# Optimization experiments

Hardware: AMD Instinct MI355X
Metric: run time of the kernel (lower is better)

## Reference

```python
import jax, jax.numpy as jnp
import numpy as np

N = 50000
E = 800000
EPS = 1e-12


def sage_conv(x, src, dst, W_l, b_l, W_r):
    # PyG SAGEConv (mean aggr): out = lin_l(mean_{j in N(i)} x_j) + lin_r(x_i)
    msg = x[src]                                             # [E, d] gather
    agg = jax.ops.segment_sum(msg, dst, num_segments=N)      # [N, d]
    cnt = jax.ops.segment_sum(jnp.ones((E,), x.dtype), dst, num_segments=N)
    mean = agg / jnp.maximum(cnt, 1.0)[:, None]              # isolated nodes -> 0
    return mean @ W_l + b_l + x @ W_r


def setup_inputs() -> dict:
    key = jax.random.key(0)
    ks = jax.random.split(key, 12)
    s = 0.05
    return {
        "x": jax.random.normal(ks[0], (N, 128), dtype=jnp.float32),
        "edge_index": jax.random.randint(ks[1], (2, E), 0, N, dtype=jnp.int64),
        # pre: Linear(128 -> 128)
        "pre_W": jax.random.normal(ks[2], (128, 128), dtype=jnp.float32) * s,
        "pre_b": jnp.zeros((128,), dtype=jnp.float32),
        # conv_first: SAGEConv(128 -> 256)
        "W1_l": jax.random.normal(ks[3], (128, 256), dtype=jnp.float32) * s,
        "b1": jnp.zeros((256,), dtype=jnp.float32),
        "W1_r": jax.random.normal(ks[4], (128, 256), dtype=jnp.float32) * s,
        # conv_hidden[0]: SAGEConv(256 -> 256)
        "W2_l": jax.random.normal(ks[5], (256, 256), dtype=jnp.float32) * s,
        "b2": jnp.zeros((256,), dtype=jnp.float32),
        "W2_r": jax.random.normal(ks[6], (256, 256), dtype=jnp.float32) * s,
        # conv_out: SAGEConv(256 -> 256)
        "W3_l": jax.random.normal(ks[7], (256, 256), dtype=jnp.float32) * s,
        "b3": jnp.zeros((256,), dtype=jnp.float32),
        "W3_r": jax.random.normal(ks[8], (256, 256), dtype=jnp.float32) * s,
    }


def reference(x, edge_index, pre_W, pre_b, W1_l, b1, W1_r, W2_l, b2, W2_r, W3_l, b3, W3_r):
    src, dst = edge_index[0], edge_index[1]
    h = x @ pre_W + pre_b                                   # feature_pre Linear
    h = jax.nn.relu(sage_conv(h, src, dst, W1_l, b1, W1_r))  # dropout = identity (eval)
    h = jax.nn.relu(sage_conv(h, src, dst, W2_l, b2, W2_r))
    h = sage_conv(h, src, dst, W3_l, b3, W3_r)
    norm = jnp.sqrt(jnp.sum(h * h, axis=-1, keepdims=True))
    return h / jnp.maximum(norm, EPS)                       # F.normalize(p=2, dim=-1)
```

## Files before the change

kernel.cpp:

```cpp
#include <hip/hip_runtime.h>
#include <cstddef>
#include <cstdint>


typedef __attribute__((ext_vector_type(8))) short short8;
typedef __attribute__((ext_vector_type(4))) float f32x4;
typedef __attribute__((ext_vector_type(2))) float f32x2;

__device__ __forceinline__ unsigned rne_bf16(float f) {
    unsigned b = __float_as_uint(f);
    return (b + 0x7fffu + ((b >> 16) & 1u)) >> 16;
}
__device__ __forceinline__ float bf16_lo(unsigned u) { return __uint_as_float(u << 16); }
__device__ __forceinline__ float bf16_hi(unsigned u) { return __uint_as_float(u & 0xffff0000u); }


__device__ __forceinline__ float dec_e4m3_sw(unsigned v) {
    unsigned s = (v & 0x80u) << 24;
    unsigned em = v & 0x7fu;
    float out;
    if (em < 8u) {
        out = (float)em * 0.001953125f;
    } else {
        out = __uint_as_float((((em >> 3) + 120u) << 23) | ((em & 7u) << 20));
    }
    return __uint_as_float(__float_as_uint(out) | s);
}

__device__ __forceinline__ unsigned char enc_e4m3(float f) {
#if __has_builtin(__builtin_amdgcn_cvt_pk_fp8_f32)
    return (unsigned char)(__builtin_amdgcn_cvt_pk_fp8_f32(f, f, 0, false) & 0xff);
#else
    unsigned b = __float_as_uint(f);
    unsigned s = (b >> 24) & 0x80u;
    unsigned a = b & 0x7fffffffu;
    if (a >= 0x43E00000u) return (unsigned char)(s | 0x7Eu);
    if (a < 0x3C800000u) {
        unsigned m = (unsigned)rintf(__uint_as_float(a) * 512.0f);
        return (unsigned char)(s | m);
    }
    unsigned r = a + 0x7FFFFu + ((a >> 20) & 1u);
    unsigned E8 = (r >> 23) - 120u;
    unsigned M = (r >> 20) & 7u;
    if (E8 > 15u || (E8 == 15u && M == 7u)) return (unsigned char)(s | 0x7Eu);
    return (unsigned char)(s | (E8 << 3) | M);
#endif
}

__device__ __forceinline__ void acc16(float* a, uint4 u) {
#if __has_builtin(__builtin_amdgcn_cvt_pk_f32_fp8)
    f32x2 f;
    f = __builtin_amdgcn_cvt_pk_f32_fp8(u.x, false); a[0] += f.x;  a[1] += f.y;
    f = __builtin_amdgcn_cvt_pk_f32_fp8(u.x, true);  a[2] += f.x;  a[3] += f.y;
    f = __builtin_amdgcn_cvt_pk_f32_fp8(u.y, false); a[4] += f.x;  a[5] += f.y;
    f = __builtin_amdgcn_cvt_pk_f32_fp8(u.y, true);  a[6] += f.x;  a[7] += f.y;
    f = __builtin_amdgcn_cvt_pk_f32_fp8(u.z, false); a[8] += f.x;  a[9] += f.y;
    f = __builtin_amdgcn_cvt_pk_f32_fp8(u.z, true);  a[10] += f.x; a[11] += f.y;
    f = __builtin_amdgcn_cvt_pk_f32_fp8(u.w, false); a[12] += f.x; a[13] += f.y;
    f = __builtin_amdgcn_cvt_pk_f32_fp8(u.w, true);  a[14] += f.x; a[15] += f.y;
#else
    unsigned d0 = u.x, d1 = u.y, d2 = u.z, d3 = u.w;
#pragma unroll
    for (int t = 0; t < 4; ++t) a[t]      += dec_e4m3_sw((d0 >> (8 * t)) & 0xffu);
#pragma unroll
    for (int t = 0; t < 4; ++t) a[4 + t]  += dec_e4m3_sw((d1 >> (8 * t)) & 0xffu);
#pragma unroll
    for (int t = 0; t < 4; ++t) a[8 + t]  += dec_e4m3_sw((d2 >> (8 * t)) & 0xffu);
#pragma unroll
    for (int t = 0; t < 4; ++t) a[12 + t] += dec_e4m3_sw((d3 >> (8 * t)) & 0xffu);
#endif
}

__device__ __forceinline__ void stage16(const void* g, unsigned short* ldsbase,
                                        int lane) {
#if __has_builtin(__builtin_amdgcn_global_load_lds)
    (void)lane;
    __builtin_amdgcn_global_load_lds(
        (const __attribute__((address_space(1))) unsigned int*)g,
        (__attribute__((address_space(3))) unsigned int*)ldsbase, 16, 0, 0);
#else
    *(uint4*)(ldsbase + (size_t)lane * 8) = *(const uint4*)g;
#endif
}


__global__ __launch_bounds__(256) void deg_kernel(const int* __restrict__ dst,
                                                  int* __restrict__ deg, int E) {
    int e = blockIdx.x * 256 + threadIdx.x;
    if (e < E) atomicAdd(&deg[dst[e]], 1);
}

__global__ __launch_bounds__(256) void bsum_kernel(const int* __restrict__ deg,
                                                   int* __restrict__ bsum, int n) {
    int i = blockIdx.x * 256 + threadIdx.x;
    int v = (i < n) ? deg[i] : 0;
#pragma unroll
    for (int s = 32; s > 0; s >>= 1) v += __shfl_down(v, s);
    __shared__ int ws[4];
    int lane = threadIdx.x & 63, w = threadIdx.x >> 6;
    if (lane == 0) ws[w] = v;
    __syncthreads();
    if (threadIdx.x == 0) bsum[blockIdx.x] = ws[0] + ws[1] + ws[2] + ws[3];
}

__global__ __launch_bounds__(256) void bscan_kernel(const int* __restrict__ bsum,
                                                    int* __restrict__ boff,
                                                    int* __restrict__ off,
                                                    int nb, int n, int E) {
    int t = threadIdx.x;
    int v = (t < nb) ? bsum[t] : 0;
    int incl = v;
#pragma unroll
    for (int s = 1; s < 64; s <<= 1) {
        int u = __shfl_up(incl, s);
        if ((t & 63) >= s) incl += u;
    }
    __shared__ int ws[4];
    int lane = t & 63, w = t >> 6;
    if (lane == 63) ws[w] = incl;
    __syncthreads();
    int woff = 0;
    for (int j = 0; j < w; ++j) woff += ws[j];
    if (t < nb) boff[t] = woff + incl - v;
    if (t == 0) off[n] = E;
}

__global__ __launch_bounds__(256) void scan_kernel(const int* __restrict__ deg,
                                                   const int* __restrict__ boff,
                                                   int* __restrict__ off,
                                                   float* __restrict__ inv, int n) {
    int i = blockIdx.x * 256 + threadIdx.x;
    int v = (i < n) ? deg[i] : 0;
    int incl = v;
#pragma unroll
    for (int s = 1; s < 64; s <<= 1) {
        int u = __shfl_up(incl, s);
        if ((threadIdx.x & 63) >= s) incl += u;
    }
    __shared__ int ws[4];
    int lane = threadIdx.x & 63, w = threadIdx.x >> 6;
    if (lane == 63) ws[w] = incl;
    __syncthreads();
    int woff = 0;
    for (int j = 0; j < w; ++j) woff += ws[j];
    if (i < n) {
        off[i] = boff[blockIdx.x] + woff + incl - v;
        inv[i] = 1.0f / fmaxf((float)v, 1.0f);
    }
}


__global__ __launch_bounds__(256) void prep_all(
    const float* __restrict__ x, uint2* __restrict__ xb, int n4, int XB,
    const float* __restrict__ pre_W, const float* __restrict__ W1_l,
    const float* __restrict__ W1_r, const float* __restrict__ W2_l,
    const float* __restrict__ W2_r, const float* __restrict__ W3_l,
    const float* __restrict__ W3_r,
    unsigned short* __restrict__ WT0, unsigned short* __restrict__ WT1,
    unsigned short* __restrict__ WT2, unsigned short* __restrict__ WT3,
    unsigned short* __restrict__ WT4, unsigned short* __restrict__ WT5,
    unsigned short* __restrict__ WT6) {
    if (blockIdx.x < (unsigned)XB) {
        int i = blockIdx.x * 256 + threadIdx.x;
        if (i >= n4) return;
        float4 v = ((const float4*)x)[i];
        uint2 o;
        o.x = rne_bf16(v.x) | (rne_bf16(v.y) << 16);
        o.y = rne_bf16(v.z) | (rne_bf16(v.w) << 16);
        xb[i] = o;
        return;
    }
    int idx = (blockIdx.x - XB) * 256 + threadIdx.x;
    if (idx < 16384) {
        int k = idx >> 7, n = idx & 127;
        WT0[n * 128 + k] = (unsigned short)rne_bf16(pre_W[idx]);
        return;
    }
    idx -= 16384;
    if (idx < 32768) {
        int k = idx >> 8, n = idx & 255;
        WT1[n * 128 + k] = (unsigned short)rne_bf16(W1_l[idx]);
        return;
    }
    idx -= 32768;
    if (idx < 32768) {
        int k = idx >> 8, n = idx & 255;
        WT2[n * 128 + k] = (unsigned short)rne_bf16(W1_r[idx]);
        return;
    }
    idx -= 32768;
    if (idx < 65536) {
        int k = idx >> 8, n = idx & 255;
        WT3[n * 256 + k] = (unsigned short)rne_bf16(W2_l[idx]);
        return;
    }
    idx -= 65536;
    if (idx < 65536) {
        int k = idx >> 8, n = idx & 255;
        WT4[n * 256 + k] = (unsigned short)rne_bf16(W2_r[idx]);
        return;
    }
    idx -= 65536;
    if (idx < 65536) {
        int k = idx >> 8, n = idx & 255;
        WT5[n * 256 + k] = (unsigned short)rne_bf16(W3_l[idx]);
        return;
    }
    idx -= 65536;
    if (idx < 65536) {
        int k = idx >> 8, n = idx & 255;
        WT6[n * 256 + k] = (unsigned short)rne_bf16(W3_r[idx]);
    }
}


template <int D>
__global__ __launch_bounds__(256) void gather_b(const unsigned short* __restrict__ h,
                                                const int* __restrict__ off,
                                                const int* __restrict__ ssrc,
                                                const float* __restrict__ inv,
                                                unsigned short* __restrict__ agg, int n) {
    int node = blockIdx.x * 4 + (threadIdx.x >> 6);
    if (node >= n) return;
    int lane = threadIdx.x & 63;
    int beg = off[node], end = off[node + 1];
    float sc = inv[node];

    const int q   = lane >> 4;
    const int sub = lane & 15;
    const unsigned short* col = h + (sub << 3);
    float a[8] = {0, 0, 0, 0, 0, 0, 0, 0};
    float b[8] = {0, 0, 0, 0, 0, 0, 0, 0};
    int k = beg;
    for (; k + 7 < end; k += 8) {
        int s0 = ssrc[k + q];
        int s1 = ssrc[k + 4 + q];
        uint4 u = *(const uint4*)(col + (size_t)s0 * D);
        uint4 v = *(const uint4*)(col + (size_t)s1 * D);
        a[0] += bf16_lo(u.x); a[1] += bf16_hi(u.x);
        a[2] += bf16_lo(u.y); a[3] += bf16_hi(u.y);
        a[4] += bf16_lo(u.z); a[5] += bf16_hi(u.z);
        a[6] += bf16_lo(u.w); a[7] += bf16_hi(u.w);
        b[0] += bf16_lo(v.x); b[1] += bf16_hi(v.x);
        b[2] += bf16_lo(v.y); b[3] += bf16_hi(v.y);
        b[4] += bf16_lo(v.z); b[5] += bf16_hi(v.z);
        b[6] += bf16_lo(v.w); b[7] += bf16_hi(v.w);
    }
    for (; k < end; k += 4) {
        int e = k + q;
        if (e < end) {
            uint4 u = *(const uint4*)(col + (size_t)ssrc[e] * D);
            a[0] += bf16_lo(u.x); a[1] += bf16_hi(u.x);
            a[2] += bf16_lo(u.y); a[3] += bf16_hi(u.y);
            a[4] += bf16_lo(u.z); a[5] += bf16_hi(u.z);
            a[6] += bf16_lo(u.w); a[7] += bf16_hi(u.w);
        }
    }
#pragma unroll
    for (int i = 0; i < 8; ++i) a[i] += b[i];
#pragma unroll
    for (int i = 0; i < 8; ++i) a[i] += __shfl_xor(a[i], 16);
#pragma unroll
    for (int i = 0; i < 8; ++i) a[i] += __shfl_xor(a[i], 32);
    if (q == 0) {
#pragma unroll
        for (int i = 0; i < 8; ++i) a[i] *= sc;
        uint4 o;
        o.x = rne_bf16(a[0]) | (rne_bf16(a[1]) << 16);
        o.y = rne_bf16(a[2]) | (rne_bf16(a[3]) << 16);
        o.z = rne_bf16(a[4]) | (rne_bf16(a[5]) << 16);
        o.w = rne_bf16(a[6]) | (rne_bf16(a[7]) << 16);
        *(uint4*)(agg + (size_t)node * D + (sub << 3)) = o;
    }
}


__global__ __launch_bounds__(256) void gather8(const unsigned char* __restrict__ h8,
                                               const int* __restrict__ off,
                                               const int* __restrict__ ssrc,
                                               const float* __restrict__ inv,
                                               unsigned short* __restrict__ agg, int n) {
    int node = blockIdx.x * 4 + (threadIdx.x >> 6);
    if (node >= n) return;
    int lane = threadIdx.x & 63;
    const int q   = lane >> 4;
    const int sub = lane & 15;
    int beg = off[node], end = off[node + 1];
    float sc = inv[node];
    const unsigned char* col = h8 + (sub << 4);

    float a[16], b[16];
#pragma unroll
    for (int i = 0; i < 16; ++i) { a[i] = 0.f; b[i] = 0.f; }

    int k = beg;
    for (; k + 7 < end; k += 8) {
        int s0 = ssrc[k + q];
        int s1 = ssrc[k + 4 + q];
        uint4 u = *(const uint4*)(col + (size_t)s0 * 256);
        uint4 v = *(const uint4*)(col + (size_t)s1 * 256);
        acc16(a, u);
        acc16(b, v);
    }
    for (; k < end; k += 4) {
        int e = k + q;
        if (e < end) {
            uint4 u = *(const uint4*)(col + (size_t)ssrc[e] * 256);
            acc16(a, u);
        }
    }
#pragma unroll
    for (int i = 0; i < 16; ++i) a[i] += b[i];
#pragma unroll
    for (int i = 0; i < 16; ++i) a[i] += __shfl_xor(a[i], 16);
#pragma unroll
    for (int i = 0; i < 16; ++i) a[i] += __shfl_xor(a[i], 32);
    if (q == 0) {
#pragma unroll
        for (int i = 0; i < 16; ++i) a[i] *= sc;
        uint4 o1, o2;
        o1.x = rne_bf16(a[0])  | (rne_bf16(a[1])  << 16);
        o1.y = rne_bf16(a[2])  | (rne_bf16(a[3])  << 16);
        o1.z = rne_bf16(a[4])  | (rne_bf16(a[5])  << 16);
        o1.w = rne_bf16(a[6])  | (rne_bf16(a[7])  << 16);
        o2.x = rne_bf16(a[8])  | (rne_bf16(a[9])  << 16);
        o2.y = rne_bf16(a[10]) | (rne_bf16(a[11]) << 16);
        o2.z = rne_bf16(a[12]) | (rne_bf16(a[13]) << 16);
        o2.w = rne_bf16(a[14]) | (rne_bf16(a[15]) << 16);
        *(uint4*)(agg + (size_t)node * 256 + (sub << 4)) = o1;
        *(uint4*)(agg + (size_t)node * 256 + (sub << 4) + 8) = o2;
    }
}


__global__ __launch_bounds__(256) void fatB(
    const unsigned short* __restrict__ xb, const unsigned short* __restrict__ WT0,
    const float* __restrict__ pre_b, unsigned short* __restrict__ h0b, int M,
    int GB,
    const int* __restrict__ src, const int* __restrict__ dst,
    const int* __restrict__ off, int* __restrict__ deg,
    int* __restrict__ ssrc, int E) {
    __shared__ __align__(16) unsigned short As[64 * 64];

    if (blockIdx.x >= (unsigned)GB) {
        int e = (blockIdx.x - GB) * 256 + threadIdx.x;
        if (e >= E) return;
        int d = dst[e];
        int pos = off[d] + atomicSub(&deg[d], 1) - 1;
        ssrc[pos] = src[e];
        return;
    }

    const int t = threadIdx.x;
    const int lane = t & 63;
    const int w = t >> 6;
    const int wm = w >> 1, wn = w & 1;
    const int m0 = blockIdx.x * 64;
    const int K = 128;

    f32x4 acc[2][4];
#pragma unroll
    for (int i = 0; i < 2; ++i)
#pragma unroll
        for (int j = 0; j < 4; ++j) acc[i][j] = (f32x4){0.f, 0.f, 0.f, 0.f};

    for (int k0 = 0; k0 < K; k0 += 64) {
#pragma unroll
        for (int i = 0; i < 2; ++i) {
            int base = (w * 2 + i) * 64;
            int p = base + lane;
            int row = p >> 3, slot = p & 7;
            int c = slot ^ (row & 7);
            int gm = m0 + row;
            if (gm >= M) gm = M - 1;
            stage16(xb + (size_t)gm * K + k0 + c * 8, &As[(size_t)base * 8], lane);
        }
        __syncthreads();
#pragma unroll
        for (int kk = 0; kk < 2; ++kk) {
            int ac = kk * 4 + (lane >> 4);
            short8 af[2], bfr[4];
#pragma unroll
            for (int i = 0; i < 2; ++i) {
                int arow = wm * 32 + i * 16 + (lane & 15);
                af[i] = *(const short8*)&As[arow * 64 + ((ac ^ (arow & 7)) << 3)];
            }
#pragma unroll
            for (int i = 0; i < 4; ++i) {
                int brow = wn * 64 + i * 16 + (lane & 15);
                bfr[i] = *(const short8*)(WT0 + (size_t)brow * K + k0 + ac * 8);
            }
#pragma unroll
            for (int mi = 0; mi < 2; ++mi)
#pragma unroll
                for (int ni = 0; ni < 4; ++ni)
                    acc[mi][ni] = __builtin_amdgcn_mfma_f32_16x16x32_bf16(
                        af[mi], bfr[ni], acc[mi][ni], 0, 0, 0);
        }
        __syncthreads();
    }

#pragma unroll
    for (int ni = 0; ni < 4; ++ni) {
        int n = wn * 64 + ni * 16 + (lane & 15);
        float bv = pre_b[n];
#pragma unroll
        for (int mi = 0; mi < 2; ++mi) {
            int mbase = m0 + wm * 32 + mi * 16 + ((lane >> 4) << 2);
#pragma unroll
            for (int r = 0; r < 4; ++r) {
                int m = mbase + r;
                if (m >= M) continue;
                h0b[(size_t)m * 128 + n] = (unsigned short)rne_bf16(acc[mi][ni][r] + bv);
            }
        }
    }
}

__global__ __launch_bounds__(256) void gemm_wide(
    const unsigned short* __restrict__ A1, const unsigned short* __restrict__ W1T,
    const unsigned short* __restrict__ A2, const unsigned short* __restrict__ W2T,
    const float* __restrict__ bias,
    unsigned short* __restrict__ outb, unsigned char* __restrict__ out8,
    float* __restrict__ outf, int M, int K, int relu) {
    __shared__ __align__(16) unsigned short As[64 * 64];
    __shared__ float rs[64][4];

    const int t = threadIdx.x;
    const int lane = t & 63;
    const int w = t >> 6;
    const int m0 = blockIdx.x * 64;

    f32x4 acc[4][4];
#pragma unroll
    for (int i = 0; i < 4; ++i)
#pragma unroll
        for (int j = 0; j < 4; ++j) acc[i][j] = (f32x4){0.f, 0.f, 0.f, 0.f};

    for (int pass = 0; pass < 2; ++pass) {
        const unsigned short* A = pass ? A2 : A1;
        const unsigned short* W = pass ? W2T : W1T;

        for (int k0 = 0; k0 < K; k0 += 64) {
#pragma unroll
            for (int i = 0; i < 2; ++i) {
                int base = (w * 2 + i) * 64;
                int p = base + lane;
                int row = p >> 3, slot = p & 7;
                int c = slot ^ (row & 7);
                int gm = m0 + row;
                if (gm >= M) gm = M - 1;
                stage16(A + (size_t)gm * K + k0 + c * 8, &As[(size_t)base * 8], lane);
            }
            __syncthreads();
#pragma unroll
            for (int kk = 0; kk < 2; ++kk) {
                int ac = kk * 4 + (lane >> 4);
                short8 af[4], bfr[4];
#pragma unroll
                for (int i = 0; i < 4; ++i) {
                    int arow = i * 16 + (lane & 15);
                    af[i] = *(const short8*)&As[arow * 64 + ((ac ^ (arow & 7)) << 3)];
                    int brow = w * 64 + i * 16 + (lane & 15);
                    bfr[i] = *(const short8*)(W + (size_t)brow * K + k0 + ac * 8);
                }
#pragma unroll
                for (int mi = 0; mi < 4; ++mi)
#pragma unroll
                    for (int ni = 0; ni < 4; ++ni)
                        acc[mi][ni] = __builtin_amdgcn_mfma_f32_16x16x32_bf16(
                            af[mi], bfr[ni], acc[mi][ni], 0, 0, 0);
            }
            __syncthreads();
        }
    }

    if (outb) {
#pragma unroll
        for (int ni = 0; ni < 4; ++ni) {
            int n = w * 64 + ni * 16 + (lane & 15);
            float bv = bias[n];
#pragma unroll
            for (int mi = 0; mi < 4; ++mi) {
                int mbase = m0 + mi * 16 + ((lane >> 4) << 2);
#pragma unroll
                for (int r = 0; r < 4; ++r) {
                    int m = mbase + r;
                    if (m >= M) continue;
                    float v = acc[mi][ni][r] + bv;
                    if (relu) v = fmaxf(v, 0.0f);
                    outb[(size_t)m * 256 + n] = (unsigned short)rne_bf16(v);
                    if (out8) out8[(size_t)m * 256 + n] = enc_e4m3(v);
                }
            }
        }
        return;
    }

#pragma unroll
    for (int ni = 0; ni < 4; ++ni) {
        float bv = bias[w * 64 + ni * 16 + (lane & 15)];
#pragma unroll
        for (int mi = 0; mi < 4; ++mi)
#pragma unroll
            for (int r = 0; r < 4; ++r) acc[mi][ni][r] += bv;
    }
#pragma unroll
    for (int mi = 0; mi < 4; ++mi) {
#pragma unroll
        for (int r = 0; r < 4; ++r) {
            float p = acc[mi][0][r] * acc[mi][0][r] + acc[mi][1][r] * acc[mi][1][r] +
                      acc[mi][2][r] * acc[mi][2][r] + acc[mi][3][r] * acc[mi][3][r];
            p += __shfl_xor(p, 1);
            p += __shfl_xor(p, 2);
            p += __shfl_xor(p, 4);
            p += __shfl_xor(p, 8);
            if ((lane & 15) == 0)
                rs[mi * 16 + ((lane >> 4) << 2) + r][w] = p;
        }
    }
    __syncthreads();
#pragma unroll
    for (int mi = 0; mi < 4; ++mi) {
        int lrow0 = mi * 16 + ((lane >> 4) << 2);
#pragma unroll
        for (int r = 0; r < 4; ++r) {
            int m = m0 + lrow0 + r;
            if (m >= M) continue;
            float s = rs[lrow0 + r][0] + rs[lrow0 + r][1] + rs[lrow0 + r][2] + rs[lrow0 + r][3];
            float sc = 1.0f / fmaxf(sqrtf(s), 1e-12f);
#pragma unroll
            for (int ni = 0; ni < 4; ++ni) {
                int n = w * 64 + ni * 16 + (lane & 15);
                outf[(size_t)m * 256 + n] = acc[mi][ni][r] * sc;
            }
        }
    }
}

extern "C" void kernel_launch(void* const* d_in, const int* in_sizes, int n_in,
                              void* d_out, int out_size, void* d_ws, size_t ws_size,
                              hipStream_t stream) {
    const int N = 50000;
    const int E = 800000;
    const int NB = (N + 255) / 256;

    const float* x     = (const float*)d_in[0];
    const int*   ei    = (const int*)d_in[1];
    const float* pre_W = (const float*)d_in[2];
    const float* pre_b = (const float*)d_in[3];
    const float* W1_l  = (const float*)d_in[4];
    const float* b1    = (const float*)d_in[5];
    const float* W1_r  = (const float*)d_in[6];
    const float* W2_l  = (const float*)d_in[7];
    const float* b2    = (const float*)d_in[8];
    const float* W2_r  = (const float*)d_in[9];
    const float* W3_l  = (const float*)d_in[10];
    const float* b3    = (const float*)d_in[11];
    const float* W3_r  = (const float*)d_in[12];
    float* out = (float*)d_out;

    const int* src = ei;
    const int* dst = ei + E;

    int* deg  = (int*)d_ws;
    int* off  = deg + N;
    int* bsum = off + N + 1;
    int* boff = bsum + 256;
    int* ssrc = boff + 256;
    size_t int_words = (size_t)2 * N + 1 + 512 + E;
    int_words = (int_words + 3) & ~(size_t)3;

    float* inv = (float*)d_ws + int_words;
    unsigned short* us = (unsigned short*)(inv + N);

    unsigned short* xb  = us;                 us += (size_t)N * 128;
    unsigned short* WT0 = us;                 us += 16384;
    unsigned short* WT1 = us;                 us += 32768;
    unsigned short* WT2 = us;                 us += 32768;
    unsigned short* WT3 = us;                 us += 65536;
    unsigned short* WT4 = us;                 us += 65536;
    unsigned short* WT5 = us;                 us += 65536;
    unsigned short* WT6 = us;                 us += 65536;
    unsigned short* h0b   = us;               us += (size_t)N * 128;
    unsigned short* agg1b = us;               us += (size_t)N * 128;
    unsigned short* h1b   = us;               us += (size_t)N * 256;
    unsigned short* agg2b = us;               us += (size_t)N * 256;
    unsigned short* h2b   = us;               us += (size_t)N * 256;
    unsigned short* agg3b = us;               us += (size_t)N * 256;
    unsigned char* h1f8 = (unsigned char*)us;
    unsigned char* h2f8 = h1f8 + (size_t)N * 256;

    hipMemsetAsync(deg, 0, (size_t)N * sizeof(int), stream);
    deg_kernel<<<(E + 255) / 256, 256, 0, stream>>>(dst, deg, E);
    bsum_kernel<<<NB, 256, 0, stream>>>(deg, bsum, N);
    bscan_kernel<<<1, 256, 0, stream>>>(bsum, boff, off, NB, N, E);
    scan_kernel<<<NB, 256, 0, stream>>>(deg, boff, off, inv, N);

    const int n4 = N * 128 / 4;
    const int XB = (n4 + 255) / 256;
    const int WB = (344064 + 255) / 256;
    prep_all<<<XB + WB, 256, 0, stream>>>(x, (uint2*)xb, n4, XB,
                                          pre_W, W1_l, W1_r, W2_l, W2_r, W3_l,
                                          W3_r, WT0, WT1, WT2, WT3, WT4, WT5, WT6);

    const int MT2 = (N + 63) / 64;
    const int AG = (N + 3) / 4;
    const int DB = (E + 255) / 256;

    fatB<<<MT2 + DB, 256, 0, stream>>>(xb, WT0, pre_b, h0b, N, MT2,
                                       src, dst, off, deg, ssrc, E);

    gather_b<128><<<AG, 256, 0, stream>>>(h0b, off, ssrc, inv, agg1b, N);
    gemm_wide<<<MT2, 256, 0, stream>>>(agg1b, WT1, h0b, WT2, b1,
                                       h1b, h1f8, nullptr, N, 128, 1);

    gather8<<<AG, 256, 0, stream>>>(h1f8, off, ssrc, inv, agg2b, N);
    gemm_wide<<<MT2, 256, 0, stream>>>(agg2b, WT3, h1b, WT4, b2,
                                       h2b, h2f8, nullptr, N, 256, 1);

    gather8<<<AG, 256, 0, stream>>>(h2f8, off, ssrc, inv, agg3b, N);
    gemm_wide<<<MT2, 256, 0, stream>>>(agg3b, WT5, h2b, WT6, b3,
                                       nullptr, nullptr, out, N, 256, 0);
}
```

Measured before the change: 496.7 us.

## Fuse degree count into prep, use 16-bit CSR indices, LDS-stage weights in wider GEMM

Three unrelated changes. The degree-count atomics move into the bf16 prep kernel, saving one launch. The CSR source indices are stored as 16-bit values, halving index traffic in the gather kernels; this is exact only because N=50000 fits in 16 bits. gemm_wide now uses 512-thread blocks over 128 rows and stages weight tiles into LDS instead of reading them from global memory per wave. The trade is more LDS per block and fewer blocks in flight.

```diff
diff --git a/kernel.cpp b/kernel.cpp
--- a/kernel.cpp
+++ b/kernel.cpp
@@ -84,12 +84,6 @@
 }
 
 
-__global__ __launch_bounds__(256) void deg_kernel(const int* __restrict__ dst,
-                                                  int* __restrict__ deg, int E) {
-    int e = blockIdx.x * 256 + threadIdx.x;
-    if (e < E) atomicAdd(&deg[dst[e]], 1);
-}
-
 __global__ __launch_bounds__(256) void bsum_kernel(const int* __restrict__ deg,
                                                    int* __restrict__ bsum, int n) {
     int i = blockIdx.x * 256 + threadIdx.x;
@@ -150,8 +144,8 @@
 }
 
 
-__global__ __launch_bounds__(256) void prep_all(
-    const float* __restrict__ x, uint2* __restrict__ xb, int n4, int XB,
+__global__ __launch_bounds__(256) void fatA(
+    const float* __restrict__ x, uint2* __restrict__ xb, int n4, int XB, int PB,
     const float* __restrict__ pre_W, const float* __restrict__ W1_l,
     const float* __restrict__ W1_r, const float* __restrict__ W2_l,
     const float* __restrict__ W2_r, const float* __restrict__ W3_l,
@@ -159,7 +153,13 @@
     unsigned short* __restrict__ WT0, unsigned short* __restrict__ WT1,
     unsigned short* __restrict__ WT2, unsigned short* __restrict__ WT3,
     unsigned short* __restrict__ WT4, unsigned short* __restrict__ WT5,
-    unsigned short* __restrict__ WT6) {
+    unsigned short* __restrict__ WT6,
+    const int* __restrict__ dst, int* __restrict__ deg, int E) {
+    if (blockIdx.x >= (unsigned)PB) {
+        int e = (blockIdx.x - PB) * 256 + threadIdx.x;
+        if (e < E) atomicAdd(&deg[dst[e]], 1);
+        return;
+    }
     if (blockIdx.x < (unsigned)XB) {
         int i = blockIdx.x * 256 + threadIdx.x;
         if (i >= n4) return;
@@ -217,7 +217,7 @@
 template <int D>
 __global__ __launch_bounds__(256) void gather_b(const unsigned short* __restrict__ h,
                                                 const int* __restrict__ off,
-                                                const int* __restrict__ ssrc,
+                                                const unsigned short* __restrict__ ssrc16,
                                                 const float* __restrict__ inv,
                                                 unsigned short* __restrict__ agg, int n) {
     int node = blockIdx.x * 4 + (threadIdx.x >> 6);
@@ -233,8 +233,8 @@
     float b[8] = {0, 0, 0, 0, 0, 0, 0, 0};
     int k = beg;
     for (; k + 7 < end; k += 8) {
-        int s0 = ssrc[k + q];
-        int s1 = ssrc[k + 4 + q];
+        int s0 = ssrc16[k + q];
+        int s1 = ssrc16[k + 4 + q];
         uint4 u = *(const uint4*)(col + (size_t)s0 * D);
         uint4 v = *(const uint4*)(col + (size_t)s1 * D);
         a[0] += bf16_lo(u.x); a[1] += bf16_hi(u.x);
@@ -249,7 +249,7 @@
     for (; k < end; k += 4) {
         int e = k + q;
         if (e < end) {
-            uint4 u = *(const uint4*)(col + (size_t)ssrc[e] * D);
+            uint4 u = *(const uint4*)(col + (size_t)ssrc16[e] * D);
             a[0] += bf16_lo(u.x); a[1] += bf16_hi(u.x);
             a[2] += bf16_lo(u.y); a[3] += bf16_hi(u.y);
             a[4] += bf16_lo(u.z); a[5] += bf16_hi(u.z);
@@ -277,7 +277,7 @@
 
 __global__ __launch_bounds__(256) void gather8(const unsigned char* __restrict__ h8,
                                                const int* __restrict__ off,
-                                               const int* __restrict__ ssrc,
+                                               const unsigned short* __restrict__ ssrc16,
                                                const float* __restrict__ inv,
                                                unsigned short* __restrict__ agg, int n) {
     int node = blockIdx.x * 4 + (threadIdx.x >> 6);
@@ -295,8 +295,8 @@
 
     int k = beg;
     for (; k + 7 < end; k += 8) {
-        int s0 = ssrc[k + q];
-        int s1 = ssrc[k + 4 + q];
+        int s0 = ssrc16[k + q];
+        int s1 = ssrc16[k + 4 + q];
         uint4 u = *(const uint4*)(col + (size_t)s0 * 256);
         uint4 v = *(const uint4*)(col + (size_t)s1 * 256);
         acc16(a, u);
@@ -305,7 +305,7 @@
     for (; k < end; k += 4) {
         int e = k + q;
         if (e < end) {
-            uint4 u = *(const uint4*)(col + (size_t)ssrc[e] * 256);
+            uint4 u = *(const uint4*)(col + (size_t)ssrc16[e] * 256);
             acc16(a, u);
         }
     }
@@ -339,7 +339,7 @@
     int GB,
     const int* __restrict__ src, const int* __restrict__ dst,
     const int* __restrict__ off, int* __restrict__ deg,
-    int* __restrict__ ssrc, int E) {
+    unsigned short* __restrict__ ssrc16, int E) {
     __shared__ __align__(16) unsigned short As[64 * 64];
 
     if (blockIdx.x >= (unsigned)GB) {
@@ -347,7 +347,7 @@
         if (e >= E) return;
         int d = dst[e];
         int pos = off[d] + atomicSub(&deg[d], 1) - 1;
-        ssrc[pos] = src[e];
+        ssrc16[pos] = (unsigned short)src[e];
         return;
     }
 
@@ -417,19 +417,21 @@
     }
 }
 
-__global__ __launch_bounds__(256) void gemm_wide(
+__global__ __launch_bounds__(512) void gemm_wide(
     const unsigned short* __restrict__ A1, const unsigned short* __restrict__ W1T,
     const unsigned short* __restrict__ A2, const unsigned short* __restrict__ W2T,
     const float* __restrict__ bias,
     unsigned short* __restrict__ outb, unsigned char* __restrict__ out8,
     float* __restrict__ outf, int M, int K, int relu) {
-    __shared__ __align__(16) unsigned short As[64 * 64];
-    __shared__ float rs[64][4];
+    __shared__ __align__(16) unsigned short As[128 * 64];
+    __shared__ __align__(16) unsigned short Bs[256 * 64];
+    __shared__ float rs[128][4];
 
     const int t = threadIdx.x;
     const int lane = t & 63;
-    const int w = t >> 6;
-    const int m0 = blockIdx.x * 64;
+    const int w8 = t >> 6;
+    const int wm = w8 >> 2, wn = w8 & 3;
+    const int m0 = blockIdx.x * 128;
 
     f32x4 acc[4][4];
 #pragma unroll
@@ -444,7 +446,7 @@
         for (int k0 = 0; k0 < K; k0 += 64) {
 #pragma unroll
             for (int i = 0; i < 2; ++i) {
-                int base = (w * 2 + i) * 64;
+                int base = (w8 * 2 + i) * 64;
                 int p = base + lane;
                 int row = p >> 3, slot = p & 7;
                 int c = slot ^ (row & 7);
@@ -452,17 +454,25 @@
                 if (gm >= M) gm = M - 1;
                 stage16(A + (size_t)gm * K + k0 + c * 8, &As[(size_t)base * 8], lane);
             }
+#pragma unroll
+            for (int i = 0; i < 4; ++i) {
+                int base = (w8 * 4 + i) * 64;
+                int p = base + lane;
+                int row = p >> 3, slot = p & 7;
+                int c = slot ^ (row & 7);
+                stage16(W + (size_t)row * K + k0 + c * 8, &Bs[(size_t)base * 8], lane);
+            }
             __syncthreads();
 #pragma unroll
             for (int kk = 0; kk < 2; ++kk) {
+                short8 af[4], bfr[4];
                 int ac = kk * 4 + (lane >> 4);
-                short8 af[4], bfr[4];
 #pragma unroll
                 for (int i = 0; i < 4; ++i) {
-                    int arow = i * 16 + (lane & 15);
+                    int arow = wm * 64 + i * 16 + (lane & 15);
                     af[i] = *(const short8*)&As[arow * 64 + ((ac ^ (arow & 7)) << 3)];
-                    int brow = w * 64 + i * 16 + (lane & 15);
-                    bfr[i] = *(const short8*)(W + (size_t)brow * K + k0 + ac * 8);
+                    int brow = wn * 64 + i * 16 + (lane & 15);
+                    bfr[i] = *(const short8*)&Bs[brow * 64 + ((ac ^ (brow & 7)) << 3)];
                 }
 #pragma unroll
                 for (int mi = 0; mi < 4; ++mi)
@@ -478,11 +488,11 @@
     if (outb) {
 #pragma unroll
         for (int ni = 0; ni < 4; ++ni) {
-            int n = w * 64 + ni * 16 + (lane & 15);
+            int n = wn * 64 + ni * 16 + (lane & 15);
             float bv = bias[n];
 #pragma unroll
             for (int mi = 0; mi < 4; ++mi) {
-                int mbase = m0 + mi * 16 + ((lane >> 4) << 2);
+                int mbase = m0 + wm * 64 + mi * 16 + ((lane >> 4) << 2);
 #pragma unroll
                 for (int r = 0; r < 4; ++r) {
                     int m = mbase + r;
@@ -499,7 +509,7 @@
 
 #pragma unroll
     for (int ni = 0; ni < 4; ++ni) {
-        float bv = bias[w * 64 + ni * 16 + (lane & 15)];
+        float bv = bias[wn * 64 + ni * 16 + (lane & 15)];
 #pragma unroll
         for (int mi = 0; mi < 4; ++mi)
 #pragma unroll
@@ -516,22 +526,23 @@
             p += __shfl_xor(p, 4);
             p += __shfl_xor(p, 8);
             if ((lane & 15) == 0)
-                rs[mi * 16 + ((lane >> 4) << 2) + r][w] = p;
+                rs[wm * 64 + mi * 16 + ((lane >> 4) << 2) + r][wn] = p;
         }
     }
     __syncthreads();
 #pragma unroll
     for (int mi = 0; mi < 4; ++mi) {
-        int lrow0 = mi * 16 + ((lane >> 4) << 2);
+        int mbase = m0 + wm * 64 + mi * 16 + ((lane >> 4) << 2);
+        int lrow = wm * 64 + mi * 16 + ((lane >> 4) << 2);
 #pragma unroll
         for (int r = 0; r < 4; ++r) {
-            int m = m0 + lrow0 + r;
+            int m = mbase + r;
             if (m >= M) continue;
-            float s = rs[lrow0 + r][0] + rs[lrow0 + r][1] + rs[lrow0 + r][2] + rs[lrow0 + r][3];
+            float s = rs[lrow + r][0] + rs[lrow + r][1] + rs[lrow + r][2] + rs[lrow + r][3];
             float sc = 1.0f / fmaxf(sqrtf(s), 1e-12f);
 #pragma unroll
             for (int ni = 0; ni < 4; ++ni) {
-                int n = w * 64 + ni * 16 + (lane & 15);
+                int n = wn * 64 + ni * 16 + (lane & 15);
                 outf[(size_t)m * 256 + n] = acc[mi][ni][r] * sc;
             }
         }
@@ -567,8 +578,8 @@
     int* off  = deg + N;
     int* bsum = off + N + 1;
     int* boff = bsum + 256;
-    int* ssrc = boff + 256;
-    size_t int_words = (size_t)2 * N + 1 + 512 + E;
+    unsigned short* ssrc16 = (unsigned short*)(boff + 256);
+    size_t int_words = (size_t)2 * N + 1 + 512 + E / 2;
     int_words = (int_words + 3) & ~(size_t)3;
 
     float* inv = (float*)d_ws + int_words;
@@ -591,35 +602,36 @@
     unsigned char* h1f8 = (unsigned char*)us;
     unsigned char* h2f8 = h1f8 + (size_t)N * 256;
 
+    const int n4 = N * 128 / 4;
+    const int XB = (n4 + 255) / 256;
+    const int WB = (344064 + 255) / 256;
+    const int PB = XB + WB;
+    const int DB = (E + 255) / 256;
+    const int MT  = (N + 127) / 128;
+    const int MT2 = (N + 63) / 64;
+    const int AG = (N + 3) / 4;
+
     hipMemsetAsync(deg, 0, (size_t)N * sizeof(int), stream);
-    deg_kernel<<<(E + 255) / 256, 256, 0, stream>>>(dst, deg, E);
+    fatA<<<PB + DB, 256, 0, stream>>>(x, (uint2*)xb, n4, XB, PB,
+                                      pre_W, W1_l, W1_r, W2_l, W2_r, W3_l, W3_r,
+                                      WT0, WT1, WT2, WT3, WT4, WT5, WT6,
+                                      dst, deg, E);
     bsum_kernel<<<NB, 256, 0, stream>>>(deg, bsum, N);
     bscan_kernel<<<1, 256, 0, stream>>>(bsum, boff, off, NB, N, E);
     scan_kernel<<<NB, 256, 0, stream>>>(deg, boff, off, inv, N);
 
-    const int n4 = N * 128 / 4;
-    const int XB = (n4 + 255) / 256;
-    const int WB = (344064 + 255) / 256;
-    prep_all<<<XB + WB, 256, 0, stream>>>(x, (uint2*)xb, n4, XB,
-                                          pre_W, W1_l, W1_r, W2_l, W2_r, W3_l,
-                                          W3_r, WT0, WT1, WT2, WT3, WT4, WT5, WT6);
-
-    const int MT2 = (N + 63) / 64;
-    const int AG = (N + 3) / 4;
-    const int DB = (E + 255) / 256;
-
     fatB<<<MT2 + DB, 256, 0, stream>>>(xb, WT0, pre_b, h0b, N, MT2,
-                                       src, dst, off, deg, ssrc, E);
-
-    gather_b<128><<<AG, 256, 0, stream>>>(h0b, off, ssrc, inv, agg1b, N);
-    gemm_wide<<<MT2, 256, 0, stream>>>(agg1b, WT1, h0b, WT2, b1,
-                                       h1b, h1f8, nullptr, N, 128, 1);
-
-    gather8<<<AG, 256, 0, stream>>>(h1f8, off, ssrc, inv, agg2b, N);
-    gemm_wide<<<MT2, 256, 0, stream>>>(agg2b, WT3, h1b, WT4, b2,
-                                       h2b, h2f8, nullptr, N, 256, 1);
-
-    gather8<<<AG, 256, 0, stream>>>(h2f8, off, ssrc, inv, agg3b, N);
-    gemm_wide<<<MT2, 256, 0, stream>>>(agg3b, WT5, h2b, WT6, b3,
-                                       nullptr, nullptr, out, N, 256, 0);
-}
+                                       src, dst, off, deg, ssrc16, E);
+
+    gather_b<128><<<AG, 256, 0, stream>>>(h0b, off, ssrc16, inv, agg1b, N);
+    gemm_wide<<<MT, 512, 0, stream>>>(agg1b, WT1, h0b, WT2, b1,
+                                      h1b, h1f8, nullptr, N, 128, 1);
+
+    gather8<<<AG, 256, 0, stream>>>(h1f8, off, ssrc16, inv, agg2b, N);
+    gemm_wide<<<MT, 512, 0, stream>>>(agg2b, WT3, h1b, WT4, b2,
+                                      h2b, h2f8, nullptr, N, 256, 1);
+
+    gather8<<<AG, 256, 0, stream>>>(h2f8, off, ssrc16, inv, agg3b, N);
+    gemm_wide<<<MT, 512, 0, stream>>>(agg3b, WT5, h2b, WT6, b3,
+                                      nullptr, nullptr, out, N, 256, 0);
+}
```

New measurement: 456.9 us. 8.0% less time.
